# Kernel optimization log

Hardware: AMD Instinct MI355X
Metric: run time of the kernel (lower is better)

Reference implementation:

```python
import jax, jax.numpy as jnp
import numpy as np


def _directional_scan(x_steps, alpha_b, reverse):
    """x_steps: (S, B, C, L); alpha_b: (1, C, 1). Returns (S, B, C, L).
    Recurrence: cur = relu(x_s + alpha * prev), prev0 = 0  (equivalent to the
    original's first-step special case since alpha*0 == 0)."""
    def step(prev, xs):
        cur = jax.nn.relu(xs + alpha_b * prev)
        return cur, cur
    init = jnp.zeros_like(x_steps[0])
    _, ys = jax.lax.scan(step, init, x_steps, reverse=reverse)
    return ys


def setup_inputs() -> dict:
    key = jax.random.key(0)
    k1, k2 = jax.random.split(key)
    B, C, H, W = 8, 32, 256, 256
    x = jax.random.normal(k1, (B, C, H, W), dtype=jnp.float32)
    alpha = jnp.full((C,), 0.2, dtype=jnp.float32)
    return {"x": x, "alpha": alpha}


def reference(x, alpha):
    # x: (B, C, H, W); alpha: (C,)
    alpha_b = alpha.reshape(1, -1, 1)  # broadcast over (B, C, L)
    x_h = jnp.moveaxis(x, 2, 0)  # (H, B, C, W)
    h_td = jnp.moveaxis(_directional_scan(x_h, alpha_b, reverse=False), 0, 2)
    h_dt = jnp.moveaxis(_directional_scan(x_h, alpha_b, reverse=True), 0, 2)
    x_w = jnp.moveaxis(x, 3, 0)  # (W, B, C, H)
    h_lr = jnp.moveaxis(_directional_scan(x_w, alpha_b, reverse=False), 0, 3)
    h_rl = jnp.moveaxis(_directional_scan(x_w, alpha_b, reverse=True), 0, 3)
    return (h_td, h_lr, h_dt, h_rl)
```

## Files before the change

kernel.cpp:

```cpp
#include <hip/hip_runtime.h>

#define BB 8
#define CC 32
#define HH 256
#define WW 256
#define SLAB 32
#define NSLAB (HH/SLAB)
#define NPLANE (BB*CC)
#define NBLK (NPLANE*NSLAB)
#define PLANE (HH*WW)
#define TS 257
#define HALO 16
#define SEG 32
#define NSEG (WW/SEG)

typedef float floatx4 __attribute__((ext_vector_type(4)));

__device__ __forceinline__ int loff(int col) {
  return (((col >> 2) + ((col & 3) << 4)) & 63) + ((col & 3) << 6);
}

__global__ __launch_bounds__(256, 4) void vscan_kernel(
    const float* __restrict__ x, const float* __restrict__ alpha,
    float* __restrict__ otd, float* __restrict__ odt) {
  const int bid = blockIdx.x;
  const int wid = (bid & 7) * (NBLK / 8) + (bid >> 3);
  const int rg = wid & (NSLAB - 1);
  const int plane = wid >> 3;
  const float a = alpha[plane & (CC - 1)];
  const int t = threadIdx.x;

  const size_t pb = (size_t)plane * PLANE;
  const float* xp = x + pb + (size_t)rg * SLAB * WW + t;
  float* ptd = otd + pb + (size_t)rg * SLAB * WW + t;
  float* pdt = odt + pb + (size_t)rg * SLAB * WW + t;

  float xr[SLAB];
#pragma unroll
  for (int i = 0; i < SLAB; ++i) xr[i] = xp[i * WW];

  float prev = 0.f;
  if (rg > 0) {
    const float* hp = x + pb + (size_t)(rg * SLAB - HALO) * WW + t;
#pragma unroll
    for (int i = 0; i < HALO; ++i)
      prev = fmaxf(fmaf(a, prev, hp[i * WW]), 0.f);
  }
#pragma unroll
  for (int i = 0; i < SLAB; ++i) {
    prev = fmaxf(fmaf(a, prev, xr[i]), 0.f);
    __builtin_nontemporal_store(prev, &ptd[i * WW]);
  }

  prev = 0.f;
  if (rg < NSLAB - 1) {
    const float* hp = x + pb + (size_t)(rg * SLAB + SLAB) * WW + t;
#pragma unroll
    for (int i = HALO - 1; i >= 0; --i)
      prev = fmaxf(fmaf(a, prev, hp[i * WW]), 0.f);
  }
#pragma unroll
  for (int i = SLAB - 1; i >= 0; --i) {
    prev = fmaxf(fmaf(a, prev, xr[i]), 0.f);
    __builtin_nontemporal_store(prev, &pdt[i * WW]);
  }
}

__global__ __launch_bounds__(256, 4) void hscan_kernel(
    const float* __restrict__ x, const float* __restrict__ alpha,
    float* __restrict__ olr, float* __restrict__ orl) {
  __shared__ float tile[SLAB * TS];

  const int bid = blockIdx.x;
  const int wid = (bid & 7) * (NBLK / 8) + (bid >> 3);
  const int rg = wid & (NSLAB - 1);
  const int plane = wid >> 3;
  const float a = alpha[plane & (CC - 1)];
  const int t = threadIdx.x;

  const size_t pbase = (size_t)plane * PLANE + (size_t)rg * SLAB * WW;
  const float* xp = x + pbase;
  float* plr = olr + pbase;
  float* prl = orl + pbase;

  const int r4 = t >> 6;
  const int c4 = t & 63;

#pragma unroll
  for (int i = 0; i < 8; ++i) {
    int row = i * 4 + r4;
    float4 v = ((const float4*)(xp + row * WW))[c4];
    float* rp = &tile[row * TS];
    rp[((c4 +  0) & 63) +   0] = v.x;
    rp[((c4 + 16) & 63) +  64] = v.y;
    rp[((c4 + 32) & 63) + 128] = v.z;
    rp[((c4 + 48) & 63) + 192] = v.w;
  }
  __syncthreads();

  const int r = t & (SLAB - 1);
  const int s = t >> 5;
  const int c0 = s << 5;
  const float* rp = &tile[r * TS];
  float xr[SEG];
#pragma unroll
  for (int j = 0; j < SEG; ++j) xr[j] = rp[loff(c0 + j)];
  float prev_lr = 0.f, prev_rl = 0.f;
  if (s > 0) {
#pragma unroll
    for (int cc = c0 - HALO; cc < c0; ++cc)
      prev_lr = fmaxf(fmaf(a, prev_lr, rp[loff(cc)]), 0.f);
  }
  if (s < NSEG - 1) {
#pragma unroll
    for (int cc = c0 + SEG + HALO - 1; cc >= c0 + SEG; --cc)
      prev_rl = fmaxf(fmaf(a, prev_rl, rp[loff(cc)]), 0.f);
  }
  __syncthreads();

  float* wp = &tile[r * TS];
#pragma unroll
  for (int j = 0; j < SEG; ++j) {
    prev_lr = fmaxf(fmaf(a, prev_lr, xr[j]), 0.f);
    wp[loff(c0 + j)] = prev_lr;
  }
  __syncthreads();

#pragma unroll
  for (int i = 0; i < 8; ++i) {
    int row = i * 4 + r4;
    const float* sp = &tile[row * TS];
    floatx4 v;
    v.x = sp[((c4 +  0) & 63) +   0];
    v.y = sp[((c4 + 16) & 63) +  64];
    v.z = sp[((c4 + 32) & 63) + 128];
    v.w = sp[((c4 + 48) & 63) + 192];
    __builtin_nontemporal_store(v, (floatx4*)(plr + row * WW) + c4);
  }
  __syncthreads();

#pragma unroll
  for (int j = SEG - 1; j >= 0; --j) {
    prev_rl = fmaxf(fmaf(a, prev_rl, xr[j]), 0.f);
    wp[loff(c0 + j)] = prev_rl;
  }
  __syncthreads();

#pragma unroll
  for (int i = 0; i < 8; ++i) {
    int row = i * 4 + r4;
    const float* sp = &tile[row * TS];
    floatx4 v;
    v.x = sp[((c4 +  0) & 63) +   0];
    v.y = sp[((c4 + 16) & 63) +  64];
    v.z = sp[((c4 + 32) & 63) + 128];
    v.w = sp[((c4 + 48) & 63) + 192];
    __builtin_nontemporal_store(v, (floatx4*)(prl + row * WW) + c4);
  }
}

extern "C" void kernel_launch(void* const* d_in, const int* in_sizes, int n_in,
                              void* d_out, int out_size, void* d_ws, size_t ws_size,
                              hipStream_t stream) {
  const float* x = (const float*)d_in[0];
  const float* alpha = (const float*)d_in[1];
  float* out = (float*)d_out;
  const size_t N = (size_t)BB * CC * HH * WW;
  float* out_td = out;
  float* out_lr = out + N;
  float* out_dt = out + 2 * N;
  float* out_rl = out + 3 * N;

  vscan_kernel<<<NBLK, 256, 0, stream>>>(x, alpha, out_td, out_dt);
  hscan_kernel<<<NBLK, 256, 0, stream>>>(x, alpha, out_lr, out_rl);
}
```

Before: 319.6 us.

## Fuse vertical and horizontal scans into one kernel with 64-row slabs

Merges the vertical and horizontal scan kernels into one kernel that loads each 64-row slab of x into shared memory once and produces all four directional outputs from it. Vertical scans read the slab from LDS instead of re-reading it from global memory, and every output is written through coalesced float4 stores from the tile. This removes one full read of the input and a kernel launch. In exchange it uses more LDS and registers per block (launch bounds drop to 2 blocks per CU), halves the block count, adds more barriers, and still fetches halo rows from global memory.

Result: faster. 313.2 us (-2.0%).

```diff
diff --git a/kernel.cpp b/kernel.cpp
--- a/kernel.cpp
+++ b/kernel.cpp
@@ -4,15 +4,14 @@
 #define CC 32
 #define HH 256
 #define WW 256
-#define SLAB 32
+#define SLAB 64
 #define NSLAB (HH/SLAB)
 #define NPLANE (BB*CC)
 #define NBLK (NPLANE*NSLAB)
 #define PLANE (HH*WW)
 #define TS 257
 #define HALO 16
-#define SEG 32
-#define NSEG (WW/SEG)
+#define SEG 64
 
 typedef float floatx4 __attribute__((ext_vector_type(4)));
 
@@ -20,74 +19,27 @@
   return (((col >> 2) + ((col & 3) << 4)) & 63) + ((col & 3) << 6);
 }
 
-__global__ __launch_bounds__(256, 4) void vscan_kernel(
+__global__ __launch_bounds__(256, 2) void fused_kernel(
     const float* __restrict__ x, const float* __restrict__ alpha,
-    float* __restrict__ otd, float* __restrict__ odt) {
+    float* __restrict__ otd, float* __restrict__ olr,
+    float* __restrict__ odt, float* __restrict__ orl) {
+  __shared__ float tile[SLAB * TS];
+
   const int bid = blockIdx.x;
   const int wid = (bid & 7) * (NBLK / 8) + (bid >> 3);
   const int rg = wid & (NSLAB - 1);
-  const int plane = wid >> 3;
+  const int plane = wid >> 2;
   const float a = alpha[plane & (CC - 1)];
   const int t = threadIdx.x;
 
-  const size_t pb = (size_t)plane * PLANE;
-  const float* xp = x + pb + (size_t)rg * SLAB * WW + t;
-  float* ptd = otd + pb + (size_t)rg * SLAB * WW + t;
-  float* pdt = odt + pb + (size_t)rg * SLAB * WW + t;
-
-  float xr[SLAB];
-#pragma unroll
-  for (int i = 0; i < SLAB; ++i) xr[i] = xp[i * WW];
-
-  float prev = 0.f;
-  if (rg > 0) {
-    const float* hp = x + pb + (size_t)(rg * SLAB - HALO) * WW + t;
-#pragma unroll
-    for (int i = 0; i < HALO; ++i)
-      prev = fmaxf(fmaf(a, prev, hp[i * WW]), 0.f);
-  }
-#pragma unroll
-  for (int i = 0; i < SLAB; ++i) {
-    prev = fmaxf(fmaf(a, prev, xr[i]), 0.f);
-    __builtin_nontemporal_store(prev, &ptd[i * WW]);
-  }
-
-  prev = 0.f;
-  if (rg < NSLAB - 1) {
-    const float* hp = x + pb + (size_t)(rg * SLAB + SLAB) * WW + t;
-#pragma unroll
-    for (int i = HALO - 1; i >= 0; --i)
-      prev = fmaxf(fmaf(a, prev, hp[i * WW]), 0.f);
-  }
-#pragma unroll
-  for (int i = SLAB - 1; i >= 0; --i) {
-    prev = fmaxf(fmaf(a, prev, xr[i]), 0.f);
-    __builtin_nontemporal_store(prev, &pdt[i * WW]);
-  }
-}
-
-__global__ __launch_bounds__(256, 4) void hscan_kernel(
-    const float* __restrict__ x, const float* __restrict__ alpha,
-    float* __restrict__ olr, float* __restrict__ orl) {
-  __shared__ float tile[SLAB * TS];
-
-  const int bid = blockIdx.x;
-  const int wid = (bid & 7) * (NBLK / 8) + (bid >> 3);
-  const int rg = wid & (NSLAB - 1);
-  const int plane = wid >> 3;
-  const float a = alpha[plane & (CC - 1)];
-  const int t = threadIdx.x;
-
   const size_t pbase = (size_t)plane * PLANE + (size_t)rg * SLAB * WW;
   const float* xp = x + pbase;
-  float* plr = olr + pbase;
-  float* prl = orl + pbase;
 
   const int r4 = t >> 6;
   const int c4 = t & 63;
 
 #pragma unroll
-  for (int i = 0; i < 8; ++i) {
+  for (int i = 0; i < 16; ++i) {
     int row = i * 4 + r4;
     float4 v = ((const float4*)(xp + row * WW))[c4];
     float* rp = &tile[row * TS];
@@ -98,64 +50,150 @@
   }
   __syncthreads();
 
-  const int r = t & (SLAB - 1);
-  const int s = t >> 5;
-  const int c0 = s << 5;
-  const float* rp = &tile[r * TS];
+  const int r = t & 63;
+  const int s = t >> 6;
+  const int c0 = s << 6;
   float xr[SEG];
-#pragma unroll
-  for (int j = 0; j < SEG; ++j) xr[j] = rp[loff(c0 + j)];
+  {
+    const float* rp = &tile[r * TS];
+#pragma unroll
+    for (int j = 0; j < SEG; ++j) xr[j] = rp[loff(c0 + j)];
+  }
   float prev_lr = 0.f, prev_rl = 0.f;
   if (s > 0) {
+    const float* rp = &tile[r * TS];
 #pragma unroll
     for (int cc = c0 - HALO; cc < c0; ++cc)
       prev_lr = fmaxf(fmaf(a, prev_lr, rp[loff(cc)]), 0.f);
   }
-  if (s < NSEG - 1) {
+  if (s < 3) {
+    const float* rp = &tile[r * TS];
 #pragma unroll
     for (int cc = c0 + SEG + HALO - 1; cc >= c0 + SEG; --cc)
       prev_rl = fmaxf(fmaf(a, prev_rl, rp[loff(cc)]), 0.f);
   }
   __syncthreads();
 
-  float* wp = &tile[r * TS];
-#pragma unroll
-  for (int j = 0; j < SEG; ++j) {
-    prev_lr = fmaxf(fmaf(a, prev_lr, xr[j]), 0.f);
-    wp[loff(c0 + j)] = prev_lr;
-  }
-  __syncthreads();
-
-#pragma unroll
-  for (int i = 0; i < 8; ++i) {
-    int row = i * 4 + r4;
-    const float* sp = &tile[row * TS];
-    floatx4 v;
-    v.x = sp[((c4 +  0) & 63) +   0];
-    v.y = sp[((c4 + 16) & 63) +  64];
-    v.z = sp[((c4 + 32) & 63) + 128];
-    v.w = sp[((c4 + 48) & 63) + 192];
-    __builtin_nontemporal_store(v, (floatx4*)(plr + row * WW) + c4);
-  }
-  __syncthreads();
-
-#pragma unroll
-  for (int j = SEG - 1; j >= 0; --j) {
-    prev_rl = fmaxf(fmaf(a, prev_rl, xr[j]), 0.f);
-    wp[loff(c0 + j)] = prev_rl;
-  }
-  __syncthreads();
-
-#pragma unroll
-  for (int i = 0; i < 8; ++i) {
-    int row = i * 4 + r4;
-    const float* sp = &tile[row * TS];
-    floatx4 v;
-    v.x = sp[((c4 +  0) & 63) +   0];
-    v.y = sp[((c4 + 16) & 63) +  64];
-    v.z = sp[((c4 + 32) & 63) + 128];
-    v.w = sp[((c4 + 48) & 63) + 192];
-    __builtin_nontemporal_store(v, (floatx4*)(prl + row * WW) + c4);
+  {
+    float* wp = &tile[r * TS];
+#pragma unroll
+    for (int j = 0; j < SEG; ++j) {
+      prev_lr = fmaxf(fmaf(a, prev_lr, xr[j]), 0.f);
+      wp[loff(c0 + j)] = prev_lr;
+    }
+  }
+  __syncthreads();
+  {
+    float* plr = olr + pbase;
+#pragma unroll
+    for (int i = 0; i < 16; ++i) {
+      int row = i * 4 + r4;
+      const float* sp = &tile[row * TS];
+      floatx4 v;
+      v.x = sp[((c4 +  0) & 63) +   0];
+      v.y = sp[((c4 + 16) & 63) +  64];
+      v.z = sp[((c4 + 32) & 63) + 128];
+      v.w = sp[((c4 + 48) & 63) + 192];
+      __builtin_nontemporal_store(v, (floatx4*)(plr + row * WW) + c4);
+    }
+  }
+  __syncthreads();
+
+  {
+    float* wp = &tile[r * TS];
+#pragma unroll
+    for (int j = SEG - 1; j >= 0; --j) {
+      prev_rl = fmaxf(fmaf(a, prev_rl, xr[j]), 0.f);
+      wp[loff(c0 + j)] = prev_rl;
+    }
+  }
+  __syncthreads();
+  {
+    float* prl = orl + pbase;
+#pragma unroll
+    for (int i = 0; i < 16; ++i) {
+      int row = i * 4 + r4;
+      const float* sp = &tile[row * TS];
+      floatx4 v;
+      v.x = sp[((c4 +  0) & 63) +   0];
+      v.y = sp[((c4 + 16) & 63) +  64];
+      v.z = sp[((c4 + 32) & 63) + 128];
+      v.w = sp[((c4 + 48) & 63) + 192];
+      __builtin_nontemporal_store(v, (floatx4*)(prl + row * WW) + c4);
+    }
+  }
+  __syncthreads();
+
+  {
+    float* wp = &tile[r * TS];
+#pragma unroll
+    for (int j = 0; j < SEG; ++j) wp[loff(c0 + j)] = xr[j];
+  }
+  __syncthreads();
+
+  const int lb = loff(t);
+  float xc[SLAB];
+  {
+    float prev = 0.f;
+    if (rg > 0) {
+      const float* hp = x + (size_t)plane * PLANE + (size_t)(rg * SLAB - HALO) * WW + t;
+#pragma unroll
+      for (int i = 0; i < HALO; ++i)
+        prev = fmaxf(fmaf(a, prev, hp[i * WW]), 0.f);
+    }
+#pragma unroll
+    for (int i = 0; i < SLAB; ++i) {
+      float xv = tile[i * TS + lb];
+      xc[i] = xv;
+      prev = fmaxf(fmaf(a, prev, xv), 0.f);
+      tile[i * TS + lb] = prev;
+    }
+  }
+  __syncthreads();
+  {
+    float* ptd = otd + pbase;
+#pragma unroll
+    for (int i = 0; i < 16; ++i) {
+      int row = i * 4 + r4;
+      const float* sp = &tile[row * TS];
+      floatx4 v;
+      v.x = sp[((c4 +  0) & 63) +   0];
+      v.y = sp[((c4 + 16) & 63) +  64];
+      v.z = sp[((c4 + 32) & 63) + 128];
+      v.w = sp[((c4 + 48) & 63) + 192];
+      __builtin_nontemporal_store(v, (floatx4*)(ptd + row * WW) + c4);
+    }
+  }
+  __syncthreads();
+
+  {
+    float prev = 0.f;
+    if (rg < NSLAB - 1) {
+      const float* hp = x + (size_t)plane * PLANE + (size_t)(rg * SLAB + SLAB) * WW + t;
+#pragma unroll
+      for (int i = HALO - 1; i >= 0; --i)
+        prev = fmaxf(fmaf(a, prev, hp[i * WW]), 0.f);
+    }
+#pragma unroll
+    for (int i = SLAB - 1; i >= 0; --i) {
+      prev = fmaxf(fmaf(a, prev, xc[i]), 0.f);
+      tile[i * TS + lb] = prev;
+    }
+  }
+  __syncthreads();
+  {
+    float* pdt = odt + pbase;
+#pragma unroll
+    for (int i = 0; i < 16; ++i) {
+      int row = i * 4 + r4;
+      const float* sp = &tile[row * TS];
+      floatx4 v;
+      v.x = sp[((c4 +  0) & 63) +   0];
+      v.y = sp[((c4 + 16) & 63) +  64];
+      v.z = sp[((c4 + 32) & 63) + 128];
+      v.w = sp[((c4 + 48) & 63) + 192];
+      __builtin_nontemporal_store(v, (floatx4*)(pdt + row * WW) + c4);
+    }
   }
 }
 
@@ -171,6 +209,5 @@
   float* out_dt = out + 2 * N;
   float* out_rl = out + 3 * N;
 
-  vscan_kernel<<<NBLK, 256, 0, stream>>>(x, alpha, out_td, out_dt);
-  hscan_kernel<<<NBLK, 256, 0, stream>>>(x, alpha, out_lr, out_rl);
+  fused_kernel<<<NBLK, 256, 0, stream>>>(x, alpha, out_td, out_lr, out_dt, out_rl);
 }
```
